# Performance work log

Measured on AMD Instinct MI355X. Metric: run time of the kernel, lower is better.

## Reference

```python
import jax, jax.numpy as jnp
import numpy as np
from jax import lax

NQ = 5  # qubits
NL = 3  # circuit layers


def conv2d(x, w, b):
    y = lax.conv_general_dilated(x, w, (1, 1), 'SAME',
                                 dimension_numbers=('NCHW', 'OIHW', 'NCHW'))
    return y + b[None, :, None, None]


def batchnorm(x, g, b, eps=1e-5):
    # training-mode batch statistics over (N,H,W), matching nn.BatchNorm2d in train()
    mu = x.mean((0, 2, 3), keepdims=True)
    var = x.var((0, 2, 3), keepdims=True)
    return g[None, :, None, None] * (x - mu) * lax.rsqrt(var + eps) + b[None, :, None, None]


def maxpool2(x):
    return lax.reduce_window(x, -jnp.inf, lax.max, (1, 1, 2, 2), (1, 1, 2, 2), 'VALID')


def _apply_1q(state, U, w):
    # state: (2,)*NQ, wire w is axis w (PennyLane default.qubit ordering)
    s = jnp.tensordot(U, state, axes=([1], [w]))
    return jnp.moveaxis(s, 0, w)


def _cnot(state, c, t):
    s0 = jnp.take(state, 0, axis=c)
    s1 = jnp.take(state, 1, axis=c)
    ta = t if t < c else t - 1
    s1 = jnp.flip(s1, axis=ta)  # X on target when control=1
    return jnp.stack([s0, s1], axis=c)


def _rx(t):
    c, s = jnp.cos(t / 2), jnp.sin(t / 2)
    return jnp.array([[c, -1j * s], [-1j * s, c]], dtype=jnp.complex64)


def _ry(t):
    c, s = jnp.cos(t / 2), jnp.sin(t / 2)
    return jnp.array([[c, -s], [s, c]], dtype=jnp.complex64)


def _rz(t):
    e = jnp.exp(-1j * t / 2)
    z = jnp.zeros((), jnp.complex64)
    return jnp.array([[e, z], [z, jnp.conj(e)]], dtype=jnp.complex64)


def quantum_circuit(inputs, weights):
    # inputs: (5,), weights: (30,)  -> scalar <Z0 Z1 Z2>
    state = jnp.zeros((2,) * NQ, jnp.complex64).at[(0,) * NQ].set(1.0)
    npl = NQ * 2  # weights per layer = 10
    nw = weights.shape[0]
    for l in range(NL):
        for i in range(NQ):
            state = _apply_1q(state, _rx(inputs[i]), i)
        for i in range(NQ):
            state = _apply_1q(state, _ry(weights[(l * npl + i) % nw]), i)
            state = _apply_1q(state, _rz(weights[(l * npl + i + NQ) % nw]), i)
        for i in range(NQ - 1):
            state = _cnot(state, i, i + 1)
        state = _cnot(state, NQ - 1, 0)
    probs = jnp.abs(state) ** 2
    z = jnp.array([1.0, -1.0], jnp.float32)
    sign = z[:, None, None] * z[None, :, None] * z[None, None, :]  # Z on wires 0,1,2
    return jnp.sum(probs * sign[:, :, :, None, None])


def setup_inputs() -> dict:
    key = jax.random.key(0)
    ks = jax.random.split(key, 12)
    d = {}
    d['x'] = jax.random.normal(ks[0], (256, 1, 224, 224), jnp.float32)
    d['conv1_w'] = jax.random.normal(ks[1], (16, 1, 3, 3), jnp.float32) * 0.1
    d['conv1_b'] = jnp.zeros((16,), jnp.float32)
    d['bn1_g'] = jnp.ones((16,), jnp.float32)
    d['bn1_b'] = jnp.zeros((16,), jnp.float32)
    d['conv2_w'] = jax.random.normal(ks[2], (32, 16, 3, 3), jnp.float32) * 0.05
    d['conv2_b'] = jnp.zeros((32,), jnp.float32)
    d['bn2_g'] = jnp.ones((32,), jnp.float32)
    d['bn2_b'] = jnp.zeros((32,), jnp.float32)
    d['conv3_w'] = jax.random.normal(ks[3], (64, 32, 3, 3), jnp.float32) * 0.05
    d['conv3_b'] = jnp.zeros((64,), jnp.float32)
    d['bn3_g'] = jnp.ones((64,), jnp.float32)
    d['bn3_b'] = jnp.zeros((64,), jnp.float32)
    d['fc1_w'] = jax.random.normal(ks[4], (64, 5), jnp.float32) * 0.1   # (in,out)
    d['fc1_b'] = jnp.zeros((5,), jnp.float32)
    d['ln_g'] = jnp.ones((5,), jnp.float32)
    d['ln_b'] = jnp.zeros((5,), jnp.float32)
    d['q_params'] = jax.random.uniform(ks[5], (30,), jnp.float32)
    d['fc2_w'] = jax.random.normal(ks[6], (1, 32), jnp.float32) * 0.5
    d['fc2_b'] = jnp.zeros((32,), jnp.float32)
    d['fc3_w'] = jax.random.normal(ks[7], (32, 2), jnp.float32) * 0.2
    d['fc3_b'] = jnp.zeros((2,), jnp.float32)
    return d


def reference(x, conv1_w, conv1_b, bn1_g, bn1_b, conv2_w, conv2_b, bn2_g, bn2_b,
              conv3_w, conv3_b, bn3_g, bn3_b, fc1_w, fc1_b, ln_g, ln_b,
              q_params, fc2_w, fc2_b, fc3_w, fc3_b):
    h = maxpool2(jax.nn.relu(batchnorm(conv2d(x, conv1_w, conv1_b), bn1_g, bn1_b)))
    h = maxpool2(jax.nn.relu(batchnorm(conv2d(h, conv2_w, conv2_b), bn2_g, bn2_b)))
    h = maxpool2(jax.nn.relu(batchnorm(conv2d(h, conv3_w, conv3_b), bn3_g, bn3_b)))
    # dropout is identity in eval; adaptive avg pool (1,1) + flatten
    h = h.mean((2, 3))                    # (B, 64)
    h = h @ fc1_w + fc1_b                 # (B, 5)
    mu = h.mean(-1, keepdims=True)
    var = h.var(-1, keepdims=True)
    h = ln_g * (h - mu) * lax.rsqrt(var + 1e-5) + ln_b
    q = jax.vmap(lambda inp: quantum_circuit(inp, q_params))(h)  # (B,)
    q = q[:, None].astype(jnp.float32)    # (B, 1)
    h2 = jax.nn.relu(q @ fc2_w + fc2_b)   # (B, 32)
    logits = h2 @ fc3_w + fc3_b           # (B, 2)
    return jax.nn.log_softmax(logits, axis=1)
```

## Files before the change

### kernel.cpp

```cpp
#include <hip/hip_runtime.h>
#include <hip/hip_bf16.h>


typedef _Float16 f16;
typedef _Float16 f16x8 __attribute__((ext_vector_type(8)));
typedef float f32x4 __attribute__((ext_vector_type(4)));

#define DEV static __device__ __forceinline__

DEV float wave_sum(float v) {
#pragma unroll
  for (int off = 32; off > 0; off >>= 1) v += __shfl_xor(v, off, 64);
  return v;
}

__global__ __launch_bounds__(256) void repack(const float* __restrict__ w2,
                                              const float* __restrict__ w3,
                                              f16* __restrict__ Bt2,
                                              f16* __restrict__ Bt3) {
  int t = blockIdx.x * 256 + threadIdx.x;
  int T = gridDim.x * 256;
  for (int i = t; i < 32 * 168; i += T) {
    int oc = i / 168, kk = i - oc * 168;
    float v = 0.f;
    if (kk < 144) {
      int tap = kk >> 4, ic = kk & 15;
      v = w2[(oc * 16 + ic) * 9 + tap];
    }
    Bt2[i] = (f16)v;
  }
  for (int i = t; i < 64 * 296; i += T) {
    int oc = i / 296, kk = i - oc * 296;
    float v = 0.f;
    if (kk < 288) {
      int tap = kk / 32, ic = kk & 31;
      v = w3[(oc * 32 + ic) * 9 + tap];
    }
    Bt3[i] = (f16)v;
  }
}

__global__ __launch_bounds__(64) void finalize(const float* __restrict__ banks,
                                               const float* __restrict__ g,
                                               const float* __restrict__ b,
                                               float* __restrict__ scsh, int C,
                                               float inv_n) {
  int c = blockIdx.x, bk = threadIdx.x;
  float s = banks[bk * 2 * C + c];
  float qq = banks[bk * 2 * C + C + c];
  s = wave_sum(s);
  qq = wave_sum(qq);
  if (bk == 0) {
    float mean = s * inv_n;
    float var = qq * inv_n - mean * mean;
    float sc = g[c] * rsqrtf(var + 1e-5f);
    scsh[c] = sc;
    scsh[C + c] = b[c] - mean * sc;
  }
}

__global__ __launch_bounds__(256) void l1_mfma(const float* __restrict__ x,
                                               const float* __restrict__ w1,
                                               float* __restrict__ banks,
                                               f16* __restrict__ h1raw) {
  __shared__ f16 xw[18 * 240];
  __shared__ f16 wB[16 * 32];
  __shared__ f16 lrow[4 * 112 * 16];
  __shared__ float lstat[32];
  int bid = blockIdx.x;
  int n = bid / 14, band = bid - n * 14;
  int y0 = band * 16;
  int t = threadIdx.x;
  if (t < 32) lstat[t] = 0.f;
  for (int i = t; i < 512; i += 256) {
    int oc = i >> 5, k = i & 31;
    wB[i] = (f16)((k < 9) ? w1[oc * 9 + k] : 0.f);
  }
  for (int i = t; i < 1008; i += 256) {
    int r = i / 56, k = i - r * 56;
    int y = y0 - 1 + r;
    float4 v = make_float4(0.f, 0.f, 0.f, 0.f);
    if ((unsigned)y < 224u)
      v = *(const float4*)(x + ((size_t)(n * 224 + y)) * 224 + k * 4);
    f16* d = xw + r * 240 + 2 + k * 4;
    d[0] = (f16)v.x; d[1] = (f16)v.y; d[2] = (f16)v.z; d[3] = (f16)v.w;
  }
  if (t < 18) {
    xw[t * 240 + 0] = (f16)0.f;
    xw[t * 240 + 1] = (f16)0.f;
    xw[t * 240 + 226] = (f16)0.f;
    xw[t * 240 + 227] = (f16)0.f;
  }
  __syncthreads();

  int wave = t >> 6, lane = t & 63, q = lane >> 4, wi = lane & 15;
  f16x8 b = *(const f16x8*)(wB + wi * 32 + q * 8);
  f16* myrow = lrow + wave * 1792;
  float ssum = 0.f, ssq = 0.f;

  for (int rp = wave; rp < 8; rp += 4) {
    for (int xt = 0; xt < 14; xt++) {
      int xi = xt * 16 + wi;
      f32x4 z4 = {0.f, 0.f, 0.f, 0.f};
      f32x4 acc0, acc1;
#pragma unroll
      for (int half = 0; half < 2; half++) {
        int lr = 2 * rp + half + 1;
        f16x8 a = {0, 0, 0, 0, 0, 0, 0, 0};
        if (q == 0) {
          const f16* r0 = xw + (lr - 1) * 240 + xi + 1;
          a[0] = r0[0]; a[1] = r0[1]; a[2] = r0[2];
          const f16* r1 = r0 + 240;
          a[3] = r1[0]; a[4] = r1[1]; a[5] = r1[2];
          const f16* r2 = r1 + 240;
          a[6] = r2[0]; a[7] = r2[1];
        } else if (q == 1) {
          a[0] = xw[(lr + 1) * 240 + xi + 3];
        }
        if (half == 0)
          acc0 = __builtin_amdgcn_mfma_f32_16x16x32_f16(a, b, z4, 0, 0, 0);
        else
          acc1 = __builtin_amdgcn_mfma_f32_16x16x32_f16(a, b, z4, 0, 0, 0);
      }
#pragma unroll
      for (int r = 0; r < 4; r++) {
        float v0 = acc0[r], v1 = acc1[r];
        ssum += v0 + v1;
        ssq += v0 * v0 + v1 * v1;
      }
      float p0 = fmaxf(fmaxf(acc0[0], acc0[1]), fmaxf(acc1[0], acc1[1]));
      float p1 = fmaxf(fmaxf(acc0[2], acc0[3]), fmaxf(acc1[2], acc1[3]));
      int pw = xt * 8 + q * 2;
      myrow[pw * 16 + wi] = (f16)p0;
      myrow[(pw + 1) * 16 + wi] = (f16)p1;
    }
    int ph = band * 8 + rp;
    f16* gdst = h1raw + ((size_t)(n * 112) + ph) * 112 * 16;
    for (int i = lane; i < 224; i += 64)
      *(f16x8*)(gdst + i * 8) = *(const f16x8*)(myrow + i * 8);
  }
  ssum += __shfl_xor(ssum, 16, 64); ssum += __shfl_xor(ssum, 32, 64);
  ssq += __shfl_xor(ssq, 16, 64);  ssq += __shfl_xor(ssq, 32, 64);
  if (q == 0) {
    atomicAdd(&lstat[wi], ssum);
    atomicAdd(&lstat[16 + wi], ssq);
  }
  __syncthreads();
  if (t < 32) atomicAdd(&banks[(bid & 63) * 32 + t], lstat[t]);
}

__global__ __launch_bounds__(256) void l2_gemm(const f16* __restrict__ h1,
                                               const f16* __restrict__ Btg,
                                               const float* __restrict__ scsh1,
                                               f16* __restrict__ p2,
                                               float* __restrict__ banks) {
  extern __shared__ char smem[];
  f16* lin = (f16*)smem;
  f16* lB = (f16*)(smem + 21888);
  f16* lpool = (f16*)(smem + 32640);
  float* lstat = (float*)(smem + 39808);
  int bid = blockIdx.x;
  int n = bid / 28, band = bid - n * 28, h0 = band * 4;
  int t = threadIdx.x;
  if (t < 64) lstat[t] = 0.f;
  {
    const uint4* s = (const uint4*)Btg;
    uint4* d = (uint4*)lB;
    for (int i = t; i < 672; i += 256) d[i] = s[i];
  }
  {
    for (int i = t; i < 1344; i += 256) {
      int r = i / 224, c = i - r * 224;
      int y = h0 + r - 1;
      f16x8 o = {0, 0, 0, 0, 0, 0, 0, 0};
      if ((unsigned)y < 112u) {
        f16x8 xv =
            *(const f16x8*)(h1 + ((size_t)(n * 112 + y)) * 112 * 16 + c * 8);
        int ch0 = (c & 1) * 8;
#pragma unroll
        for (int k = 0; k < 8; k++) {
          float f = (float)xv[k] * scsh1[ch0 + k] + scsh1[16 + ch0 + k];
          o[k] = (f16)fmaxf(f, 0.f);
        }
      }
      *(f16x8*)(lin + ((size_t)r * 228 + 2 + c) * 8) = o;
    }
    if (t < 24) {
      int r = t >> 2, k = t & 3;
      f16x8 z = {0, 0, 0, 0, 0, 0, 0, 0};
      *(f16x8*)(lin + ((size_t)r * 228 + ((k < 2) ? k : (226 + k - 2))) * 8) = z;
    }
  }
  __syncthreads();
  int wave = t >> 6, lane = t & 63, q = lane >> 4, wi = lane & 15;
  const int icq = (q & 1) * 8;
  f32x4 acc[7][2];
#pragma unroll
  for (int f = 0; f < 7; f++)
#pragma unroll
    for (int nf = 0; nf < 2; nf++)
#pragma unroll
      for (int r = 0; r < 4; r++) acc[f][nf][r] = 0.f;

#pragma unroll
  for (int j = 0; j < 5; j++) {
    const int tA = 2 * j, tB = 2 * j + 1;
    const int kyA = tA / 3, kxA = tA % 3;
    const int kyB = (tB < 9) ? tB / 3 : 0, kxB = (tB < 9) ? tB % 3 : 0;
    bool hiq = (q >= 2);
    int ky = hiq ? kyB : kyA;
    int kx = hiq ? kxB : kxA;
    const f16* aptr0 = lin + ((wave + ky) * 114 + wi + kx) * 16 + icq;
    bool zq = (j == 4) && hiq;
    const f16* zptr = lB + 152;
    f16x8 b0 = *(const f16x8*)(lB + wi * 168 + j * 32 + q * 8);
    f16x8 b1 = *(const f16x8*)(lB + (16 + wi) * 168 + j * 32 + q * 8);
#pragma unroll
    for (int f = 0; f < 7; f++) {
      const f16* ap = zq ? zptr : (aptr0 + f * 256);
      f16x8 a = *(const f16x8*)ap;
      acc[f][0] = __builtin_amdgcn_mfma_f32_16x16x32_f16(a, b0, acc[f][0], 0, 0, 0);
      acc[f][1] = __builtin_amdgcn_mfma_f32_16x16x32_f16(a, b1, acc[f][1], 0, 0, 0);
    }
  }
  float s0 = 0.f, q0 = 0.f, s1 = 0.f, q1 = 0.f;
#pragma unroll
  for (int f = 0; f < 7; f++)
#pragma unroll
    for (int r = 0; r < 4; r++) {
      float v0 = acc[f][0][r], v1 = acc[f][1][r];
      s0 += v0; q0 += v0 * v0;
      s1 += v1; q1 += v1 * v1;
    }
  s0 += __shfl_xor(s0, 16, 64); s0 += __shfl_xor(s0, 32, 64);
  q0 += __shfl_xor(q0, 16, 64); q0 += __shfl_xor(q0, 32, 64);
  s1 += __shfl_xor(s1, 16, 64); s1 += __shfl_xor(s1, 32, 64);
  q1 += __shfl_xor(q1, 16, 64); q1 += __shfl_xor(q1, 32, 64);
  if (q == 0) {
    atomicAdd(&lstat[wi], s0);
    atomicAdd(&lstat[16 + wi], s1);
    atomicAdd(&lstat[32 + wi], q0);
    atomicAdd(&lstat[48 + wi], q1);
  }
  if (wave & 1) {
#pragma unroll
    for (int f = 0; f < 7; f++)
#pragma unroll
      for (int nf = 0; nf < 2; nf++) {
        int ch = nf * 16 + wi;
        int pc0 = f * 8 + q * 2;
        float m0 = fmaxf(acc[f][nf][0], acc[f][nf][1]);
        float m1 = fmaxf(acc[f][nf][2], acc[f][nf][3]);
        lpool[((wave >> 1) * 56 + pc0) * 32 + ch] = (f16)m0;
        lpool[((wave >> 1) * 56 + pc0 + 1) * 32 + ch] = (f16)m1;
      }
  }
  __syncthreads();
  if (!(wave & 1)) {
    int ph = band * 2 + (wave >> 1);
#pragma unroll
    for (int f = 0; f < 7; f++)
#pragma unroll
      for (int nf = 0; nf < 2; nf++) {
        int ch = nf * 16 + wi;
        int pc0 = f * 8 + q * 2;
        float m0 = fmaxf(acc[f][nf][0], acc[f][nf][1]);
        float m1 = fmaxf(acc[f][nf][2], acc[f][nf][3]);
        m0 = fmaxf(m0, (float)lpool[((wave >> 1) * 56 + pc0) * 32 + ch]);
        m1 = fmaxf(m1, (float)lpool[((wave >> 1) * 56 + pc0 + 1) * 32 + ch]);
        size_t ob = (((size_t)n * 56 + ph) * 56) * 32;
        p2[ob + (size_t)pc0 * 32 + ch] = (f16)m0;
        p2[ob + (size_t)(pc0 + 1) * 32 + ch] = (f16)m1;
      }
  }
  if (t < 64) {
    int i = t >> 5, c = t & 31;
    atomicAdd(&banks[(bid & 63) * 64 + i * 32 + c], lstat[i * 32 + c]);
  }
}

__global__ __launch_bounds__(256) void l3_gemm(const f16* __restrict__ p2,
                                               const f16* __restrict__ Btg,
                                               const float* __restrict__ scsh2,
                                               f16* __restrict__ p3,
                                               float* __restrict__ banks) {
  extern __shared__ char smem[];
  f16* lin = (f16*)smem;
  f16* lB = (f16*)(smem + 22272);
  f16* lpool = (f16*)(smem + 41216);
  float* lstat = (float*)(smem + 48384);
  int bx = blockIdx.x, zo = blockIdx.y;
  int n = bx / 14, band = bx - n * 14, h0 = band * 4;
  int t = threadIdx.x;
  if (t < 64) lstat[t] = 0.f;
  {
    const uint4* s = (const uint4*)(Btg + (size_t)zo * 32 * 296);
    uint4* d = (uint4*)lB;
    for (int i = t; i < 1184; i += 256) d[i] = s[i];
  }
  {
    for (int i = t; i < 1344; i += 256) {
      int r = i / 224, rem = i - r * 224;
      int c = rem >> 2, cp = rem & 3;
      int y = h0 + r - 1;
      f16x8 o = {0, 0, 0, 0, 0, 0, 0, 0};
      if ((unsigned)y < 56u) {
        const f16* src = p2 + (((size_t)(n * 56 + y)) * 56 + c) * 32 + cp * 8;
        f16x8 xv = *(const f16x8*)src;
        int ch0 = cp * 8;
#pragma unroll
        for (int k = 0; k < 8; k++) {
          float f = (float)xv[k] * scsh2[ch0 + k] + scsh2[32 + ch0 + k];
          o[k] = (f16)fmaxf(f, 0.f);
        }
      }
      *(f16x8*)(lin + ((size_t)r * 58 + 1 + c) * 32 + cp * 8) = o;
    }
    if (t < 48) {
      int r = t / 8, k = t & 7;
      int col = (k < 4) ? 0 : 57, cp = k & 3;
      f16x8 z = {0, 0, 0, 0, 0, 0, 0, 0};
      *(f16x8*)(lin + ((size_t)r * 58 + col) * 32 + cp * 8) = z;
    }
  }
  __syncthreads();
  int wave = t >> 6, lane = t & 63, q = lane >> 4, wi = lane & 15;
  int mhalf = wave & 1, nf = wave >> 1;
  int abase[7];
#pragma unroll
  for (int f = 0; f < 7; f++) {
    int pos = mhalf * 112 + f * 16 + wi;
    int r = pos / 56, w = pos - r * 56;
    abase[f] = (r * 58 + w) * 32 + q * 8;
  }
  f32x4 acc[7];
#pragma unroll
  for (int f = 0; f < 7; f++)
#pragma unroll
    for (int r = 0; r < 4; r++) acc[f][r] = 0.f;

#pragma unroll
  for (int j = 0; j < 9; j++) {
    const int ky = j / 3, kx = j % 3;
    f16x8 b = *(const f16x8*)(lB + (nf * 16 + wi) * 296 + j * 32 + q * 8);
#pragma unroll
    for (int f = 0; f < 7; f++) {
      f16x8 a = *(const f16x8*)(lin + abase[f] + (ky * 58 + kx) * 32);
      acc[f] = __builtin_amdgcn_mfma_f32_16x16x32_f16(a, b, acc[f], 0, 0, 0);
    }
  }
  int ch_local = nf * 16 + wi;
  float s0 = 0.f, q0 = 0.f;
#pragma unroll
  for (int f = 0; f < 7; f++)
#pragma unroll
    for (int r = 0; r < 4; r++) {
      float v = acc[f][r];
      s0 += v; q0 += v * v;
    }
  s0 += __shfl_xor(s0, 16, 64); s0 += __shfl_xor(s0, 32, 64);
  q0 += __shfl_xor(q0, 16, 64); q0 += __shfl_xor(q0, 32, 64);
  if (q == 0) {
    atomicAdd(&lstat[ch_local], s0);
    atomicAdd(&lstat[32 + ch_local], q0);
  }
#pragma unroll
  for (int f = 0; f < 7; f++) {
    int pos = mhalf * 112 + f * 16 + q * 4;
    int r0 = pos / 56, w0 = pos - r0 * 56;
    int p2i = pos + 2;
    int r1 = p2i / 56, w1 = p2i - r1 * 56;
    float m0 = fmaxf(acc[f][0], acc[f][1]);
    float m1 = fmaxf(acc[f][2], acc[f][3]);
    lpool[(r0 * 28 + (w0 >> 1)) * 32 + ch_local] = (f16)m0;
    lpool[(r1 * 28 + (w1 >> 1)) * 32 + ch_local] = (f16)m1;
  }
  __syncthreads();
  for (int i = t; i < 1792; i += 256) {
    int ch = i & 31, rest = i >> 5;
    int pc = rest % 28, pr = rest / 28;
    float v = fmaxf((float)lpool[((2 * pr) * 28 + pc) * 32 + ch],
                    (float)lpool[((2 * pr + 1) * 28 + pc) * 32 + ch]);
    int gpr = band * 2 + pr;
    p3[(((size_t)n * 28 + gpr) * 28 + pc) * 64 + zo * 32 + ch] = (f16)v;
  }
  if (t < 64) {
    int i = t >> 5, c = t & 31;
    int bank = (bx * 2 + zo) & 63;
    atomicAdd(&banks[bank * 128 + i * 64 + zo * 32 + c], lstat[i * 32 + c]);
  }
}

__global__ __launch_bounds__(256) void head_pool(
    const f16* __restrict__ p3, const float* __restrict__ scsh3,
    const float* __restrict__ fc1w, const float* __restrict__ fc1b,
    float* __restrict__ featg) {
  int n = blockIdx.x, t = threadIdx.x;
  __shared__ float red[64 * 33];
  __shared__ float meanc[64];
  int oct = t & 7, strip = t >> 3;
  float sc[8], sh[8];
#pragma unroll
  for (int k = 0; k < 8; k++) {
    sc[k] = scsh3[oct * 8 + k];
    sh[k] = scsh3[64 + oct * 8 + k];
  }
  float acc[8];
#pragma unroll
  for (int k = 0; k < 8; k++) acc[k] = 0.f;
  const f16* base = p3 + (size_t)n * 50176 + oct * 8;
  for (int px = strip; px < 784; px += 32) {
    f16x8 v = *(const f16x8*)(base + (size_t)px * 64);
#pragma unroll
    for (int k = 0; k < 8; k++)
      acc[k] += fmaxf((float)v[k] * sc[k] + sh[k], 0.f);
  }
#pragma unroll
  for (int k = 0; k < 8; k++) red[(oct * 8 + k) * 33 + strip] = acc[k];
  __syncthreads();
  if (t < 64) {
    float s = 0.f;
    for (int j = 0; j < 32; j++) s += red[t * 33 + j];
    meanc[t] = s * (1.f / 784.f);
  }
  __syncthreads();
  if (t < 5) {
    float a = fc1b[t];
    for (int i = 0; i < 64; i++) a += meanc[i] * fc1w[i * 5 + t];
    featg[n * 8 + t] = a;
  }
}

template <int W>
DEV void g_rx(float (&sr)[32], float (&si)[32], float c, float s) {
  constexpr int m = 1 << (4 - W);
#pragma unroll
  for (int i0 = 0; i0 < 32; i0++)
    if (!(i0 & m)) {
      constexpr int dummy = 0; (void)dummy;
      int i1 = i0 | m;
      float a0r = sr[i0], a0i = si[i0], a1r = sr[i1], a1i = si[i1];
      sr[i0] = c * a0r + s * a1i;
      si[i0] = c * a0i - s * a1r;
      sr[i1] = s * a0i + c * a1r;
      si[i1] = -s * a0r + c * a1i;
    }
}

template <int W>
DEV void g_ry(float (&sr)[32], float (&si)[32], float c, float s) {
  constexpr int m = 1 << (4 - W);
#pragma unroll
  for (int i0 = 0; i0 < 32; i0++)
    if (!(i0 & m)) {
      int i1 = i0 | m;
      float a0r = sr[i0], a0i = si[i0], a1r = sr[i1], a1i = si[i1];
      sr[i0] = c * a0r - s * a1r;
      si[i0] = c * a0i - s * a1i;
      sr[i1] = s * a0r + c * a1r;
      si[i1] = s * a0i + c * a1i;
    }
}

template <int W>
DEV void g_rz(float (&sr)[32], float (&si)[32], float c, float s) {
  constexpr int m = 1 << (4 - W);
#pragma unroll
  for (int i0 = 0; i0 < 32; i0++)
    if (!(i0 & m)) {
      int i1 = i0 | m;
      float a0r = sr[i0], a0i = si[i0], a1r = sr[i1], a1i = si[i1];
      sr[i0] = c * a0r + s * a0i;
      si[i0] = c * a0i - s * a0r;
      sr[i1] = c * a1r - s * a1i;
      si[i1] = c * a1i + s * a1r;
    }
}

template <int C, int T>
DEV void g_cnot(float (&sr)[32], float (&si)[32]) {
  constexpr int mc = 1 << (4 - C), mt = 1 << (4 - T);
#pragma unroll
  for (int i0 = 0; i0 < 32; i0++)
    if ((i0 & mc) && !(i0 & mt)) {
      int i1 = i0 | mt;
      float tr = sr[i0]; sr[i0] = sr[i1]; sr[i1] = tr;
      float ti = si[i0]; si[i0] = si[i1]; si[i1] = ti;
    }
}

__global__ __launch_bounds__(64) void head_q(
    const float* __restrict__ featg, const float* __restrict__ lng,
    const float* __restrict__ lnb, const float* __restrict__ qp,
    const float* __restrict__ fc2w, const float* __restrict__ fc2b,
    const float* __restrict__ fc3w, const float* __restrict__ fc3b,
    float* __restrict__ out) {
  int n = blockIdx.x * 64 + threadIdx.x;
  float f[5];
#pragma unroll
  for (int i = 0; i < 5; i++) f[i] = featg[n * 8 + i];
  float mu = (f[0] + f[1] + f[2] + f[3] + f[4]) * 0.2f;
  float var = 0.f;
#pragma unroll
  for (int i = 0; i < 5; i++) { float d = f[i] - mu; var += d * d; }
  var *= 0.2f;
  float inv = rsqrtf(var + 1e-5f);
#pragma unroll
  for (int i = 0; i < 5; i++) f[i] = lng[i] * (f[i] - mu) * inv + lnb[i];

  float cx[5], sx[5];
#pragma unroll
  for (int i = 0; i < 5; i++) {
    cx[i] = cosf(0.5f * f[i]);
    sx[i] = sinf(0.5f * f[i]);
  }
  float sr[32], si[32];
#pragma unroll
  for (int i = 0; i < 32; i++) { sr[i] = 0.f; si[i] = 0.f; }
  sr[0] = 1.f;

  for (int l = 0; l < 3; l++) {
    g_rx<0>(sr, si, cx[0], sx[0]);
    g_rx<1>(sr, si, cx[1], sx[1]);
    g_rx<2>(sr, si, cx[2], sx[2]);
    g_rx<3>(sr, si, cx[3], sx[3]);
    g_rx<4>(sr, si, cx[4], sx[4]);
#define WIRE_YZ(I)                                             \
  {                                                            \
    float ty = qp[l * 10 + I];                                 \
    g_ry<I>(sr, si, cosf(0.5f * ty), sinf(0.5f * ty));         \
    float tz = qp[l * 10 + I + 5];                             \
    g_rz<I>(sr, si, cosf(0.5f * tz), sinf(0.5f * tz));         \
  }
    WIRE_YZ(0) WIRE_YZ(1) WIRE_YZ(2) WIRE_YZ(3) WIRE_YZ(4)
#undef WIRE_YZ
    g_cnot<0, 1>(sr, si);
    g_cnot<1, 2>(sr, si);
    g_cnot<2, 3>(sr, si);
    g_cnot<3, 4>(sr, si);
    g_cnot<4, 0>(sr, si);
  }
  float qv = 0.f;
#pragma unroll
  for (int idx = 0; idx < 32; idx++) {
    float p = sr[idx] * sr[idx] + si[idx] * si[idx];
    qv += (__popc(idx & 0x1C) & 1) ? -p : p;
  }
  float l0 = fc3b[0], l1 = fc3b[1];
  for (int j = 0; j < 32; j++) {
    float hv = fmaxf(qv * fc2w[j] + fc2b[j], 0.f);
    l0 += hv * fc3w[j * 2];
    l1 += hv * fc3w[j * 2 + 1];
  }
  float mx = fmaxf(l0, l1);
  float lse = mx + logf(expf(l0 - mx) + expf(l1 - mx));
  out[n * 2 + 0] = l0 - lse;
  out[n * 2 + 1] = l1 - lse;
}

extern "C" void kernel_launch(void* const* d_in, const int* in_sizes, int n_in,
                              void* d_out, int out_size, void* d_ws,
                              size_t ws_size, hipStream_t stream) {
  const float* x    = (const float*)d_in[0];
  const float* w1   = (const float*)d_in[1];
  const float* bn1g = (const float*)d_in[3];
  const float* bn1b = (const float*)d_in[4];
  const float* w2   = (const float*)d_in[5];
  const float* bn2g = (const float*)d_in[7];
  const float* bn2b = (const float*)d_in[8];
  const float* w3   = (const float*)d_in[9];
  const float* bn3g = (const float*)d_in[11];
  const float* bn3b = (const float*)d_in[12];
  const float* fc1w = (const float*)d_in[13];
  const float* fc1b = (const float*)d_in[14];
  const float* lng  = (const float*)d_in[15];
  const float* lnb  = (const float*)d_in[16];
  const float* qp   = (const float*)d_in[17];
  const float* fc2w = (const float*)d_in[18];
  const float* fc2b = (const float*)d_in[19];
  const float* fc3w = (const float*)d_in[20];
  const float* fc3b = (const float*)d_in[21];
  float* out = (float*)d_out;

  char* ws = (char*)d_ws;
  float* banks1 = (float*)ws;
  float* banks2 = (float*)(ws + 8192);
  float* banks3 = (float*)(ws + 24576);
  float* scsh1 = (float*)(ws + 57344);
  float* scsh2 = (float*)(ws + 57472);
  float* scsh3 = (float*)(ws + 57728);
  f16* Bt2 = (f16*)(ws + 58240);
  f16* Bt3 = (f16*)(ws + 68992);
  f16* h1 = (f16*)(ws + 106880);
  f16* p2 = (f16*)(ws + 106880 + 102760448ULL);
  f16* p3 = (f16*)(ws + 106880 + 102760448ULL + 51380224ULL);
  float* featg = banks2;

  hipMemsetAsync(ws, 0, 57344, stream);
  repack<<<16, 256, 0, stream>>>(w2, w3, Bt2, Bt3);
  l1_mfma<<<3584, 256, 0, stream>>>(x, w1, banks1, h1);
  finalize<<<16, 64, 0, stream>>>(banks1, bn1g, bn1b, scsh1, 16,
                                  1.f / 12845056.f);
  l2_gemm<<<7168, 256, 40064, stream>>>(h1, Bt2, scsh1, p2, banks2);
  finalize<<<32, 64, 0, stream>>>(banks2, bn2g, bn2b, scsh2, 32,
                                  1.f / 3211264.f);
  l3_gemm<<<dim3(3584, 2), 256, 48640, stream>>>(p2, Bt3, scsh2, p3, banks3);
  finalize<<<64, 64, 0, stream>>>(banks3, bn3g, bn3b, scsh3, 64,
                                  1.f / 802816.f);
  head_pool<<<256, 256, 0, stream>>>(p3, scsh3, fc1w, fc1b, featg);
  head_q<<<4, 64, 0, stream>>>(featg, lng, lnb, qp, fc2w, fc2b, fc3w, fc3b,
                               out);
}
```

Before: 414.3 us.

## Rework layer-1 conv to use 32x32x16 MFMA with dual-offset input buffers

Layer 1 conv moves from 16x16x32 MFMAs, which wasted most of the K dimension, to 32x32x16 MFMAs. Each lane packs a 2x4 input patch, and the weights are arranged so that two adjacent output rows share one MFMA. Two shifted copies of the input tile (xA, xB) keep the odd and even lane loads aligned for f16x2 reads. Max-pooling now needs a cross-lane shuffle. The point is fewer MFMA issues and less scalar gathering of the A operand, at the cost of extra LDS for the second copy and per-element shuffles in the epilogue.

Result: faster. 393.5 us (-5.0%).

```diff
diff --git a/kernel.cpp b/kernel.cpp
--- a/kernel.cpp
+++ b/kernel.cpp
@@ -3,8 +3,11 @@
 
 
 typedef _Float16 f16;
+typedef _Float16 f16x2 __attribute__((ext_vector_type(2)));
+typedef _Float16 f16x4 __attribute__((ext_vector_type(4)));
 typedef _Float16 f16x8 __attribute__((ext_vector_type(8)));
 typedef float f32x4 __attribute__((ext_vector_type(4)));
+typedef float f32x16 __attribute__((ext_vector_type(16)));
 
 #define DEV static __device__ __forceinline__
 
@@ -59,91 +62,101 @@
   }
 }
 
-__global__ __launch_bounds__(256) void l1_mfma(const float* __restrict__ x,
-                                               const float* __restrict__ w1,
-                                               float* __restrict__ banks,
-                                               f16* __restrict__ h1raw) {
-  __shared__ f16 xw[18 * 240];
-  __shared__ f16 wB[16 * 32];
-  __shared__ f16 lrow[4 * 112 * 16];
+__global__ __launch_bounds__(256) void l1_mfma32(const float* __restrict__ x,
+                                                 const float* __restrict__ w1,
+                                                 float* __restrict__ banks,
+                                                 f16* __restrict__ h1raw) {
+  __shared__ f16 xA[18 * 240];
+  __shared__ f16 xB[18 * 240];
+  __shared__ f16 lrow[4 * 1792];
   __shared__ float lstat[32];
   int bid = blockIdx.x;
   int n = bid / 14, band = bid - n * 14;
   int y0 = band * 16;
   int t = threadIdx.x;
   if (t < 32) lstat[t] = 0.f;
-  for (int i = t; i < 512; i += 256) {
-    int oc = i >> 5, k = i & 31;
-    wB[i] = (f16)((k < 9) ? w1[oc * 9 + k] : 0.f);
-  }
   for (int i = t; i < 1008; i += 256) {
     int r = i / 56, k = i - r * 56;
     int y = y0 - 1 + r;
     float4 v = make_float4(0.f, 0.f, 0.f, 0.f);
     if ((unsigned)y < 224u)
       v = *(const float4*)(x + ((size_t)(n * 224 + y)) * 224 + k * 4);
-    f16* d = xw + r * 240 + 2 + k * 4;
-    d[0] = (f16)v.x; d[1] = (f16)v.y; d[2] = (f16)v.z; d[3] = (f16)v.w;
+    f16 h0 = (f16)v.x, h1 = (f16)v.y, h2 = (f16)v.z, h3 = (f16)v.w;
+    f16* pa = xA + r * 240 + 4 * k + 1;
+    pa[0] = h0; pa[1] = h1; pa[2] = h2; pa[3] = h3;
+    f16x4 pk = {h0, h1, h2, h3};
+    *(f16x4*)(xB + r * 240 + 4 * k) = pk;
   }
   if (t < 18) {
-    xw[t * 240 + 0] = (f16)0.f;
-    xw[t * 240 + 1] = (f16)0.f;
-    xw[t * 240 + 226] = (f16)0.f;
-    xw[t * 240 + 227] = (f16)0.f;
-  }
-  __syncthreads();
-
-  int wave = t >> 6, lane = t & 63, q = lane >> 4, wi = lane & 15;
-  f16x8 b = *(const f16x8*)(wB + wi * 32 + q * 8);
+    xA[t * 240 + 0] = (f16)0.f;
+    xA[t * 240 + 225] = (f16)0.f;
+    xA[t * 240 + 226] = (f16)0.f;
+    xB[t * 240 + 224] = (f16)0.f;
+    xB[t * 240 + 225] = (f16)0.f;
+  }
+  __syncthreads();
+
+  int wave = t >> 6, lane = t & 63;
+  int g = lane >> 5, m32 = lane & 31;
+  int oc = m32 & 15, s = m32 >> 4;
+
+  f16x8 b;
+#pragma unroll
+  for (int j = 0; j < 8; j++) {
+    int ky = 2 * g + (j >> 2), kx = j & 3;
+    int kys = ky - s;
+    float wv = 0.f;
+    if (kx < 3 && kys >= 0 && kys < 3) wv = w1[oc * 9 + kys * 3 + kx];
+    b[j] = (f16)wv;
+  }
+
+  const f16* abase = (m32 & 1) ? (xB + (m32 - 1)) : (xA + m32);
   f16* myrow = lrow + wave * 1792;
+  const int bp[8] = {0, 1, 4, 5, 8, 9, 12, 13};
   float ssum = 0.f, ssq = 0.f;
 
   for (int rp = wave; rp < 8; rp += 4) {
-    for (int xt = 0; xt < 14; xt++) {
-      int xi = xt * 16 + wi;
-      f32x4 z4 = {0.f, 0.f, 0.f, 0.f};
-      f32x4 acc0, acc1;
-#pragma unroll
-      for (int half = 0; half < 2; half++) {
-        int lr = 2 * rp + half + 1;
-        f16x8 a = {0, 0, 0, 0, 0, 0, 0, 0};
-        if (q == 0) {
-          const f16* r0 = xw + (lr - 1) * 240 + xi + 1;
-          a[0] = r0[0]; a[1] = r0[1]; a[2] = r0[2];
-          const f16* r1 = r0 + 240;
-          a[3] = r1[0]; a[4] = r1[1]; a[5] = r1[2];
-          const f16* r2 = r1 + 240;
-          a[6] = r2[0]; a[7] = r2[1];
-        } else if (q == 1) {
-          a[0] = xw[(lr + 1) * 240 + xi + 3];
+    int r0 = 2 * rp + 2 * g;
+    const f16* rbase = abase + r0 * 240;
+    for (int xt = 0; xt < 7; xt++) {
+      const f16* p0 = rbase + xt * 32;
+      f16x2 v0 = *(const f16x2*)(p0);
+      f16x2 v1 = *(const f16x2*)(p0 + 2);
+      f16x2 v2 = *(const f16x2*)(p0 + 240);
+      f16x2 v3 = *(const f16x2*)(p0 + 242);
+      f16x8 a = {v0[0], v0[1], v1[0], v1[1], v2[0], v2[1], v3[0], v3[1]};
+      f32x16 z; 
+#pragma unroll
+      for (int r = 0; r < 16; r++) z[r] = 0.f;
+      f32x16 acc = __builtin_amdgcn_mfma_f32_32x32x16_f16(a, b, z, 0, 0, 0);
+#pragma unroll
+      for (int r = 0; r < 16; r++) {
+        float v = acc[r];
+        ssum += v;
+        ssq += v * v;
+      }
+#pragma unroll
+      for (int i = 0; i < 8; i++) {
+        float pm = fmaxf(acc[2 * i], acc[2 * i + 1]);
+        pm = fmaxf(pm, __shfl_xor(pm, 16, 64));
+        if (s == 0) {
+          int pxp = xt * 16 + bp[i] + 2 * g;
+          myrow[pxp * 16 + oc] = (f16)pm;
         }
-        if (half == 0)
-          acc0 = __builtin_amdgcn_mfma_f32_16x16x32_f16(a, b, z4, 0, 0, 0);
-        else
-          acc1 = __builtin_amdgcn_mfma_f32_16x16x32_f16(a, b, z4, 0, 0, 0);
       }
-#pragma unroll
-      for (int r = 0; r < 4; r++) {
-        float v0 = acc0[r], v1 = acc1[r];
-        ssum += v0 + v1;
-        ssq += v0 * v0 + v1 * v1;
-      }
-      float p0 = fmaxf(fmaxf(acc0[0], acc0[1]), fmaxf(acc1[0], acc1[1]));
-      float p1 = fmaxf(fmaxf(acc0[2], acc0[3]), fmaxf(acc1[2], acc1[3]));
-      int pw = xt * 8 + q * 2;
-      myrow[pw * 16 + wi] = (f16)p0;
-      myrow[(pw + 1) * 16 + wi] = (f16)p1;
     }
     int ph = band * 8 + rp;
     f16* gdst = h1raw + ((size_t)(n * 112) + ph) * 112 * 16;
     for (int i = lane; i < 224; i += 64)
       *(f16x8*)(gdst + i * 8) = *(const f16x8*)(myrow + i * 8);
   }
-  ssum += __shfl_xor(ssum, 16, 64); ssum += __shfl_xor(ssum, 32, 64);
-  ssq += __shfl_xor(ssq, 16, 64);  ssq += __shfl_xor(ssq, 32, 64);
-  if (q == 0) {
-    atomicAdd(&lstat[wi], ssum);
-    atomicAdd(&lstat[16 + wi], ssq);
+  ssum += __shfl_xor(ssum, 16, 64);
+  ssum += __shfl_xor(ssum, 32, 64);
+  ssq += __shfl_xor(ssq, 16, 64);
+  ssq += __shfl_xor(ssq, 32, 64);
+  if (lane < 16) {
+    atomicAdd(&lstat[oc], ssum);
+    atomicAdd(&lstat[16 + oc], ssq);
   }
   __syncthreads();
   if (t < 32) atomicAdd(&banks[(bid & 63) * 32 + t], lstat[t]);
@@ -437,7 +450,6 @@
 #pragma unroll
   for (int i0 = 0; i0 < 32; i0++)
     if (!(i0 & m)) {
-      constexpr int dummy = 0; (void)dummy;
       int i1 = i0 | m;
       float a0r = sr[i0], a0i = si[i0], a1r = sr[i1], a1i = si[i1];
       sr[i0] = c * a0r + s * a1i;
@@ -598,7 +610,7 @@
 
   hipMemsetAsync(ws, 0, 57344, stream);
   repack<<<16, 256, 0, stream>>>(w2, w3, Bt2, Bt3);
-  l1_mfma<<<3584, 256, 0, stream>>>(x, w1, banks1, h1);
+  l1_mfma32<<<3584, 256, 0, stream>>>(x, w1, banks1, h1);
   finalize<<<16, 64, 0, stream>>>(banks1, bn1g, bn1b, scsh1, 16,
                                   1.f / 12845056.f);
   l2_gemm<<<7168, 256, 40064, stream>>>(h1, Bt2, scsh1, p2, banks2);
```
